# Optimization experiments

Hardware: AMD Instinct MI355X
Metric: run time of the kernel (lower is better)

Reference implementation:

```python
import jax, jax.numpy as jnp
import numpy as np

B, C, K = 8, 32, 512


def setup_inputs() -> dict:
    key = jax.random.key(0)
    k1, k2, k3 = jax.random.split(key, 3)
    amplitude = jax.random.normal(k1, (B, C, K), dtype=jnp.float32)
    phase = jax.random.normal(k2, (B, C, K), dtype=jnp.float32)
    A = jax.random.normal(k3, (K, K), dtype=jnp.float32)
    w_amplitude = jnp.float32(0.5)
    w_phase = jnp.float32(0.5)
    return {"amplitude": amplitude, "phase": phase, "A": A,
            "w_amplitude": w_amplitude, "w_phase": w_phase}


def reference(amplitude, phase, A, w_amplitude, w_phase):
    # amplitude, phase: (B, C, K)
    # pairwise differences along the frequency axis -> (B, C, K, K)
    amp_diff = amplitude[..., :, None] - amplitude[..., None, :]
    ph_diff = phase[..., :, None] - phase[..., None, :]
    fused = w_amplitude * amp_diff + w_phase * ph_diff
    # einsum('dd,bxcd->bxcd', A, fused): scale last axis by diag(A)
    temp = fused * jnp.diagonal(A)
    # einsum('bxcd,bxcd->bcd'): sum of squares over channel axis x=C -> (B, K, K)
    dist = jnp.sum(temp * temp, axis=1)
    exp_dist = 1.0 / (dist + 1e-10)
    eye = jnp.eye(K, dtype=exp_dist.dtype)
    offdiag = 1.0 - eye
    exp_dist = exp_dist * offdiag
    exp_max = jax.lax.stop_gradient(jnp.max(exp_dist, axis=-1, keepdims=True))
    p = exp_dist / exp_max
    p = (p * offdiag + eye) * 0.99  # probabilities in (0, 0.99]
    # bernoulli gumbel-softmax (hard, tau=1) with straight-through estimator
    logit = jnp.log(p / (1.0 - p))          # log(p/(1-p)); other class is -logit
    logits = jnp.stack([logit, -logit], axis=-1)  # (B, K, K, 2)
    gkey = jax.random.key(42)
    u = jax.random.uniform(gkey, logits.shape, minval=1e-10, maxval=1.0)
    gumbel = -jnp.log(-jnp.log(u))
    y_soft = jax.nn.softmax(logits + gumbel, axis=-1)
    idx = jnp.argmax(y_soft, axis=-1)
    y_hard = jax.nn.one_hot(idx, 2, dtype=y_soft.dtype)
    y = y_hard + y_soft - jax.lax.stop_gradient(y_soft)
    sample = y[..., 0]  # (B, K, K)
    return sample.mean(axis=0)  # (K, K)
```

## Files before the change

kernel.cpp:

```cpp
#include <hip/hip_runtime.h>
#include <stdint.h>
#include <math.h>

constexpr int NB = 8;
constexpr int NC = 32;
constexpr int NK = 512;
constexpr int ROWS = 4;

__device__ __forceinline__ uint32_t rotl32(uint32_t x, uint32_t r) {
    return (x << r) | (x >> (32u - r));
}

__device__ __forceinline__ uint32_t jax_random_bits(uint32_t n) {
    const uint32_t k0 = 0u, k1 = 42u;
    const uint32_t ks2 = k0 ^ k1 ^ 0x1BD11BDAu;
    uint32_t x0 = 0u + k0, x1 = n + k1;

    x0 += x1; x1 = rotl32(x1, 13); x1 ^= x0;
    x0 += x1; x1 = rotl32(x1, 15); x1 ^= x0;
    x0 += x1; x1 = rotl32(x1, 26); x1 ^= x0;
    x0 += x1; x1 = rotl32(x1,  6); x1 ^= x0;
    x0 += k1; x1 += ks2 + 1u;

    x0 += x1; x1 = rotl32(x1, 17); x1 ^= x0;
    x0 += x1; x1 = rotl32(x1, 29); x1 ^= x0;
    x0 += x1; x1 = rotl32(x1, 16); x1 ^= x0;
    x0 += x1; x1 = rotl32(x1, 24); x1 ^= x0;
    x0 += ks2; x1 += k0 + 2u;

    x0 += x1; x1 = rotl32(x1, 13); x1 ^= x0;
    x0 += x1; x1 = rotl32(x1, 15); x1 ^= x0;
    x0 += x1; x1 = rotl32(x1, 26); x1 ^= x0;
    x0 += x1; x1 = rotl32(x1,  6); x1 ^= x0;
    x0 += k0; x1 += k1 + 3u;

    x0 += x1; x1 = rotl32(x1, 17); x1 ^= x0;
    x0 += x1; x1 = rotl32(x1, 29); x1 ^= x0;
    x0 += x1; x1 = rotl32(x1, 16); x1 ^= x0;
    x0 += x1; x1 = rotl32(x1, 24); x1 ^= x0;
    x0 += k1; x1 += ks2 + 4u;

    x0 += x1; x1 = rotl32(x1, 13); x1 ^= x0;
    x0 += x1; x1 = rotl32(x1, 15); x1 ^= x0;
    x0 += x1; x1 = rotl32(x1, 26); x1 ^= x0;
    x0 += x1; x1 = rotl32(x1,  6); x1 ^= x0;
    x0 += ks2; x1 += k0 + 5u;

    return x0 ^ x1;
}

__device__ __forceinline__ float fastL(uint32_t bits, double& ud) {
    const double S = 1.0 - 1e-10, T = 1e-10;
    uint32_t fb = (bits >> 9) | 0x3F800000u;
    float bf = __uint_as_float(fb) - 1.0f;
    ud = (double)bf * S + T;
    if (bf <= 0.5f) {
        return -logf((float)ud);
    } else {
        double vm1 = S * ((double)bf - 1.0);
        return -log1pf((float)vm1);
    }
}

__device__ __noinline__ bool decide_slow(double a2, double c2,
                                         double u0, double u1) {
    return a2 * (-log(u1)) >= c2 * (-log(u0));
}

__global__ void prep_kernel(const float* __restrict__ amp,
                            const float* __restrict__ ph,
                            const float* __restrict__ A,
                            const float* __restrict__ wav,
                            const float* __restrict__ wpv,
                            double* __restrict__ F,
                            double* __restrict__ A2,
                            float* __restrict__ out) {
    int t = blockIdx.x * 256 + threadIdx.x;
    out[t] = 0.0f;
    if (t < NB * NC * NK) {
        double wa = (double)wav[0], wp = (double)wpv[0];
        F[t] = wa * (double)amp[t] + wp * (double)ph[t];
    }
    if (t < NK) {
        double a = (double)A[t * NK + t];
        A2[t] = a * a;
    }
}

__global__ __launch_bounds__(256) void sample_kernel(
    const double* __restrict__ F, const double* __restrict__ A2,
    float* __restrict__ out)
{
    const int i0   = blockIdx.x * ROWS;
    const int b    = blockIdx.y;
    const int tid  = threadIdx.x;
    const int j0   = 2 * tid;
    const int lane = tid & 63;
    const int wv   = tid >> 6;
    const int wjb  = wv * 128;

    __shared__ double Dsh[4][ROWS][128];
    __shared__ unsigned short wlist[4][ROWS * 128];
    __shared__ double sred[ROWS][4];
    __shared__ double s_q[ROWS];

    const double* __restrict__ Fb = F + (size_t)b * NC * NK;

    double acc[2][ROWS];
    #pragma unroll
    for (int it = 0; it < 2; ++it)
        #pragma unroll
        for (int r = 0; r < ROWS; ++r) acc[it][r] = 0.0;

    #pragma unroll 8
    for (int c = 0; c < NC; ++c) {
        double fi_r[ROWS];
        #pragma unroll
        for (int r = 0; r < ROWS; ++r)
            fi_r[r] = Fb[c * NK + i0 + r];
        double2 fj = *(const double2*)(Fb + c * NK + j0);
        #pragma unroll
        for (int r = 0; r < ROWS; ++r) {
            double d0 = fi_r[r] - fj.x; acc[0][r] = fma(d0, d0, acc[0][r]);
            double d1 = fi_r[r] - fj.y; acc[1][r] = fma(d1, d1, acc[1][r]);
        }
    }

    double2 a2j = *(const double2*)(A2 + j0);
    double D[2][ROWS];
    #pragma unroll
    for (int r = 0; r < ROWS; ++r) {
        D[0][r] = acc[0][r] * a2j.x + 1e-10;
        D[1][r] = acc[1][r] * a2j.y + 1e-10;
        *(double2*)&Dsh[wv][r][2 * lane] = make_double2(D[0][r], D[1][r]);
    }

    #pragma unroll
    for (int r = 0; r < ROWS; ++r) {
        const int i = i0 + r;
        double m = 1e300;
        if (j0     != i) m = fmin(m, D[0][r]);
        if (j0 + 1 != i) m = fmin(m, D[1][r]);
        #pragma unroll
        for (int off = 32; off > 0; off >>= 1)
            m = fmin(m, __shfl_down(m, off));
        if (lane == 0) sred[r][wv] = m;
    }
    __syncthreads();
    if (tid < ROWS) {
        double m = fmin(fmin(sred[tid][0], sred[tid][1]),
                        fmin(sred[tid][2], sred[tid][3]));
        s_q[tid] = 0.99 * m;
    }
    __syncthreads();

    const unsigned long long ltmask = (1ull << lane) - 1ull;
    int nb = 0;
    #pragma unroll
    for (int r = 0; r < ROWS; ++r) {
        const int i = i0 + r;
        const double q = s_q[r];
        const double thr = 1.95e8 * (q * q);
        double t0 = D[0][r] - q;
        double t1 = D[1][r] - q;
        bool need0 = (j0     == i) || !(t0 * t0 > thr);
        bool need1 = (j0 + 1 == i) || !(t1 * t1 > thr);
        unsigned long long m0 = __ballot(need0);
        unsigned long long m1 = __ballot(need1);
        int c0 = __popcll(m0);
        if (need0) wlist[wv][nb + __popcll(m0 & ltmask)] =
            (unsigned short)((r << 8) | (2 * lane));
        if (need1) wlist[wv][nb + c0 + __popcll(m1 & ltmask)] =
            (unsigned short)((r << 8) | (2 * lane + 1));
        nb += c0 + __popcll(m1);
    }

    for (int k0v = 0; k0v < nb; k0v += 64) {
        int k = k0v + lane;
        bool act = k < nb;
        int e  = wlist[wv][act ? k : 0];
        int r  = e >> 8;
        int jl = e & 255;
        double Dv = Dsh[wv][r][jl];
        double q  = s_q[r];
        const int i = i0 + r;
        const int j = wjb + jl;

        double a2, c2;
        if (j == i) { a2 = 9801.0; c2 = 1.0; }
        else        { a2 = q * q; double t = Dv - q; c2 = t * t; }

        uint32_t n0 = 2u * (((uint32_t)(b * NK + i)) * NK + (uint32_t)j);
        bool hit = false;
        if (act) {
            uint32_t bits0 = jax_random_bits(n0);
            double u0d;
            float L0f = fastL(bits0, u0d);
            float L0lo = L0f * 0.99999f;
            if (!((double)c2 * (double)L0lo > 23.03 * a2)) {
                uint32_t bits1 = jax_random_bits(n0 + 1u);
                double u1d;
                float L1f = fastL(bits1, u1d);
                float lhs = (float)a2 * L1f;
                float rhs = (float)c2 * L0f;
                float diff = lhs - rhs;
                if (fabsf(diff) > 1e-4f * (lhs + rhs))
                    hit = diff >= 0.0f;
                else
                    hit = decide_slow(a2, c2, u0d, u1d);
            }
        }
        if (hit)
            atomicAdd(&out[i * NK + j], 0.125f);
    }
}

extern "C" void kernel_launch(void* const* d_in, const int* in_sizes, int n_in,
                              void* d_out, int out_size, void* d_ws, size_t ws_size,
                              hipStream_t stream) {
    const float* amp = (const float*)d_in[0];
    const float* ph  = (const float*)d_in[1];
    const float* A   = (const float*)d_in[2];
    const float* wa  = (const float*)d_in[3];
    const float* wp  = (const float*)d_in[4];
    float* out = (float*)d_out;

    double* F  = (double*)d_ws;
    double* A2 = (double*)d_ws + NB * NC * NK;

    prep_kernel<<<1024, 256, 0, stream>>>(amp, ph, A, wa, wp, F, A2, out);

    dim3 grid(NK / ROWS, NB);
    sample_kernel<<<grid, 256, 0, stream>>>(F, A2, out);
}
```

Before: 79.22 us.

## Split sampling into filter and decide kernels via global candidate lists

```diff
diff --git a/kernel.cpp b/kernel.cpp
--- a/kernel.cpp
+++ b/kernel.cpp
@@ -6,6 +6,9 @@
 constexpr int NC = 32;
 constexpr int NK = 512;
 constexpr int ROWS = 4;
+constexpr int SLOT = 512;
+
+struct alignas(16) Entry { uint32_t tag; uint32_t pad; double D; };
 
 __device__ __forceinline__ uint32_t rotl32(uint32_t x, uint32_t r) {
     return (x << r) | (x >> (32u - r));
@@ -87,9 +90,10 @@
     }
 }
 
-__global__ __launch_bounds__(256) void sample_kernel(
+__global__ __launch_bounds__(256) void filter_kernel(
     const double* __restrict__ F, const double* __restrict__ A2,
-    float* __restrict__ out)
+    double* __restrict__ qarr, uint32_t* __restrict__ counts,
+    Entry* __restrict__ list)
 {
     const int i0   = blockIdx.x * ROWS;
     const int b    = blockIdx.y;
@@ -97,10 +101,9 @@
     const int j0   = 2 * tid;
     const int lane = tid & 63;
     const int wv   = tid >> 6;
-    const int wjb  = wv * 128;
-
-    __shared__ double Dsh[4][ROWS][128];
-    __shared__ unsigned short wlist[4][ROWS * 128];
+    const int wid  = ((b * gridDim.x) + blockIdx.x) * 4 + wv;
+    Entry* __restrict__ slot = list + (size_t)wid * SLOT;
+
     __shared__ double sred[ROWS][4];
     __shared__ double s_q[ROWS];
 
@@ -132,7 +135,6 @@
     for (int r = 0; r < ROWS; ++r) {
         D[0][r] = acc[0][r] * a2j.x + 1e-10;
         D[1][r] = acc[1][r] * a2j.y + 1e-10;
-        *(double2*)&Dsh[wv][r][2 * lane] = make_double2(D[0][r], D[1][r]);
     }
 
     #pragma unroll
@@ -150,7 +152,9 @@
     if (tid < ROWS) {
         double m = fmin(fmin(sred[tid][0], sred[tid][1]),
                         fmin(sred[tid][2], sred[tid][3]));
-        s_q[tid] = 0.99 * m;
+        double qv = 0.99 * m;
+        s_q[tid] = qv;
+        qarr[b * NK + i0 + tid] = qv;
     }
     __syncthreads();
 
@@ -168,47 +172,60 @@
         unsigned long long m0 = __ballot(need0);
         unsigned long long m1 = __ballot(need1);
         int c0 = __popcll(m0);
-        if (need0) wlist[wv][nb + __popcll(m0 & ltmask)] =
-            (unsigned short)((r << 8) | (2 * lane));
-        if (need1) wlist[wv][nb + c0 + __popcll(m1 & ltmask)] =
-            (unsigned short)((r << 8) | (2 * lane + 1));
+        const uint32_t rowtag = (uint32_t)(b * NK + i) << 9;
+        if (need0) {
+            Entry e{rowtag | (uint32_t)j0, 0u, D[0][r]};
+            slot[nb + __popcll(m0 & ltmask)] = e;
+        }
+        if (need1) {
+            Entry e{rowtag | (uint32_t)(j0 + 1), 0u, D[1][r]};
+            slot[nb + c0 + __popcll(m1 & ltmask)] = e;
+        }
         nb += c0 + __popcll(m1);
     }
-
-    for (int k0v = 0; k0v < nb; k0v += 64) {
-        int k = k0v + lane;
-        bool act = k < nb;
-        int e  = wlist[wv][act ? k : 0];
-        int r  = e >> 8;
-        int jl = e & 255;
-        double Dv = Dsh[wv][r][jl];
-        double q  = s_q[r];
-        const int i = i0 + r;
-        const int j = wjb + jl;
+    if (lane == 0) counts[wid] = (uint32_t)nb;
+}
+
+__global__ __launch_bounds__(256) void decide_kernel(
+    const Entry* __restrict__ list, const uint32_t* __restrict__ counts,
+    const double* __restrict__ qarr, float* __restrict__ out)
+{
+    const int lane = threadIdx.x & 63;
+    const int wv   = threadIdx.x >> 6;
+    const int wid  = blockIdx.x * 4 + wv;
+    const Entry* __restrict__ slot = list + (size_t)wid * SLOT;
+    const int n = (int)counts[wid];
+
+    for (int k = lane; k < n; k += 64) {
+        Entry e = slot[k];
+        const uint32_t tag = e.tag;
+        const int j   = (int)(tag & 511u);
+        const int row = (int)(tag >> 9);
+        const int i   = row & 511;
+        const double Dv = e.D;
+        const double q  = qarr[row];
 
         double a2, c2;
         if (j == i) { a2 = 9801.0; c2 = 1.0; }
         else        { a2 = q * q; double t = Dv - q; c2 = t * t; }
 
-        uint32_t n0 = 2u * (((uint32_t)(b * NK + i)) * NK + (uint32_t)j);
+        const uint32_t n0 = 2u * ((uint32_t)row * (uint32_t)NK + (uint32_t)j);
         bool hit = false;
-        if (act) {
-            uint32_t bits0 = jax_random_bits(n0);
-            double u0d;
-            float L0f = fastL(bits0, u0d);
-            float L0lo = L0f * 0.99999f;
-            if (!((double)c2 * (double)L0lo > 23.03 * a2)) {
-                uint32_t bits1 = jax_random_bits(n0 + 1u);
-                double u1d;
-                float L1f = fastL(bits1, u1d);
-                float lhs = (float)a2 * L1f;
-                float rhs = (float)c2 * L0f;
-                float diff = lhs - rhs;
-                if (fabsf(diff) > 1e-4f * (lhs + rhs))
-                    hit = diff >= 0.0f;
-                else
-                    hit = decide_slow(a2, c2, u0d, u1d);
-            }
+        uint32_t bits0 = jax_random_bits(n0);
+        double u0d;
+        float L0f = fastL(bits0, u0d);
+        float L0lo = L0f * 0.99999f;
+        if (!((double)c2 * (double)L0lo > 23.03 * a2)) {
+            uint32_t bits1 = jax_random_bits(n0 + 1u);
+            double u1d;
+            float L1f = fastL(bits1, u1d);
+            float lhs = (float)a2 * L1f;
+            float rhs = (float)c2 * L0f;
+            float diff = lhs - rhs;
+            if (fabsf(diff) > 1e-4f * (lhs + rhs))
+                hit = diff >= 0.0f;
+            else
+                hit = decide_slow(a2, c2, u0d, u1d);
         }
         if (hit)
             atomicAdd(&out[i * NK + j], 0.125f);
@@ -225,11 +242,16 @@
     const float* wp  = (const float*)d_in[4];
     float* out = (float*)d_out;
 
-    double* F  = (double*)d_ws;
-    double* A2 = (double*)d_ws + NB * NC * NK;
+    double*   F      = (double*)d_ws;
+    double*   A2     = F + NB * NC * NK;
+    double*   qarr   = A2 + NK;
+    uint32_t* counts = (uint32_t*)(qarr + NB * NK);
+    Entry*    list   = (Entry*)((char*)counts + 4096 * sizeof(uint32_t));
 
     prep_kernel<<<1024, 256, 0, stream>>>(amp, ph, A, wa, wp, F, A2, out);
 
     dim3 grid(NK / ROWS, NB);
-    sample_kernel<<<grid, 256, 0, stream>>>(F, A2, out);
-}
+    filter_kernel<<<grid, 256, 0, stream>>>(F, A2, qarr, counts, list);
+
+    decide_kernel<<<1024, 256, 0, stream>>>(list, counts, qarr, out);
+}
```

Result: slower. 82.16 us (+3.7%).
